# Performance work log

Hardware: AMD Instinct MI355X
Metric: run time of the kernel (lower is better)

Reference implementation:

```python
import jax, jax.numpy as jnp
import numpy as np

B = 16384       # batch
H = 512         # hidden_size
OUT = 4         # output_size (== GRU input_size)
FF = 2048       # MLP hidden width
HORIZON = 5     # prediction_horizon


def setup_inputs() -> dict:
    key = jax.random.key(0)
    ks = jax.random.split(key, 12)
    s = 0.05
    f32 = jnp.float32
    return {
        "predicted_values": jax.random.normal(ks[0], (B, HORIZON, OUT), f32),
        "past_time_features": jax.random.normal(ks[1], (B, H), f32),
        # nn.GRU (single layer) params, PyTorch layout: (3H, in) / (3H, H), gate order r,z,n
        "w_ih": jax.random.normal(ks[2], (3 * H, OUT), f32) * s,
        "w_hh": jax.random.normal(ks[3], (3 * H, H), f32) * s,
        "b_ih": jax.random.normal(ks[4], (3 * H,), f32) * s,
        "b_hh": jax.random.normal(ks[5], (3 * H,), f32) * s,
        # hx_fc: Linear(2H -> H)
        "w_fc": jax.random.normal(ks[6], (H, 2 * H), f32) * s,
        "b_fc": jax.random.normal(ks[7], (H,), f32) * s,
        # mlp: Linear(H -> 2048), Linear(2048 -> OUT); Dropout is identity at eval
        "w1": jax.random.normal(ks[8], (FF, H), f32) * s,
        "b1": jax.random.normal(ks[9], (FF,), f32) * s,
        "w2": jax.random.normal(ks[10], (OUT, FF), f32) * s,
        "b2": jax.random.normal(ks[11], (OUT,), f32) * s,
    }


def _gru_cell(x, h, w_ih, w_hh, b_ih, b_hh):
    # PyTorch GRU cell: gates ordered (r, z, n)
    gi = x @ w_ih.T + b_ih          # [B, 3H]
    gh = h @ w_hh.T + b_hh          # [B, 3H]
    i_r, i_z, i_n = jnp.split(gi, 3, axis=-1)
    h_r, h_z, h_n = jnp.split(gh, 3, axis=-1)
    r = jax.nn.sigmoid(i_r + h_r)
    z = jax.nn.sigmoid(i_z + h_z)
    n = jnp.tanh(i_n + r * h_n)
    return (1.0 - z) * n + z * h


def reference(predicted_values, past_time_features, w_ih, w_hh, b_ih, b_hh,
              w_fc, b_fc, w1, b1, w2, b2):
    b = predicted_values.shape[0]
    xy = jnp.zeros((b, OUT), predicted_values.dtype)
    hx = past_time_features.reshape(b, H)
    outs = []
    for i in range(HORIZON):
        # length-2 sequence through the GRU: [xy, predicted_values[:, i]]
        h1 = _gru_cell(xy, hx, w_ih, w_hh, b_ih, b_hh)
        h2 = _gru_cell(predicted_values[:, i, :], h1, w_ih, w_hh, b_ih, b_hh)
        hcat = jnp.concatenate([h1, h2], axis=-1)        # [B, 2H]
        hx = hcat @ w_fc.T + b_fc                        # [B, H]
        # MLP: ReLU -> Linear -> (Dropout=identity) -> ReLU -> Linear
        d_xy = jax.nn.relu(jax.nn.relu(hx) @ w1.T + b1) @ w2.T + b2
        xy = xy + d_xy
        outs.append(xy)
    return jnp.stack(outs, axis=1)                       # [B, HORIZON, OUT]
```

## Files before the change

### kernel.cpp

```cpp
#include <hip/hip_runtime.h>
#include <hip/hip_bf16.h>
#include <cstdint>
#include <cstddef>

#define Bsz 16384
#define HORsz 5

using bf16_t = __hip_bfloat16;
typedef __bf16 bf16x8 __attribute__((ext_vector_type(8)));
typedef float f32x4 __attribute__((ext_vector_type(4)));

__device__ __forceinline__ void gld_lds16(const void* g, void* l) {
  __builtin_amdgcn_global_load_lds((__attribute__((address_space(1))) void*)g,
                                   (__attribute__((address_space(3))) void*)l,
                                   16, 0, 0);
}

template <int N>
__device__ __forceinline__ void wait_vmcnt() {
  if constexpr (N == 0)      asm volatile("s_waitcnt vmcnt(0)" ::: "memory");
  else if constexpr (N == 3) asm volatile("s_waitcnt vmcnt(3)" ::: "memory");
  else if constexpr (N == 4) asm volatile("s_waitcnt vmcnt(4)" ::: "memory");
  else static_assert(N == 0 || N == 3 || N == 4, "unsupported vmcnt");
}

__device__ __forceinline__ float sigm(float x) { return 1.f / (1.f + __expf(-x)); }
__device__ __forceinline__ float tanh_fast(float x) {
  x = fminf(fmaxf(x, -20.f), 20.f);
  float e = __expf(2.f * x);
  return (e - 1.f) / (e + 1.f);
}

template <int CTRL>
__device__ __forceinline__ float dpp_add(float v) {
  int x = __builtin_amdgcn_update_dpp(0, __float_as_int(v), CTRL, 0xF, 0xF, true);
  return v + __int_as_float(x);
}
__device__ __forceinline__ float red16(float v) {
  v = dpp_add<0xB1>(v);
  v = dpp_add<0x4E>(v);
  v = dpp_add<0x124>(v);
  v = dpp_add<0x128>(v);
  return v;
}

__device__ __forceinline__ void swz(int b, int nbn, int& n, int& m) {
  const int x = b & 7;
  const int k = b >> 3;
  n = k % nbn;
  m = x + 8 * (k / nbn);
}

__device__ __forceinline__ size_t fl_off(int row, int col, int ca, int cofs) {
  return (size_t)((row >> 4) * ca + cofs + (col >> 5)) * 1024
       + (size_t)((((col >> 3) & 3) * 16 + (row & 15)) * 16 + (col & 7) * 2);
}

__global__ void __launch_bounds__(256) pack_fl(const float* __restrict__ src,
                                               char* __restrict__ dst,
                                               int C, int cs, int npieces) {
  const int p = blockIdx.x * 256 + threadIdx.x;
  if (p >= npieces) return;
  const int chunk = p >> 6, wi = p & 63;
  const int colgrp = wi >> 4, r15 = wi & 15;
  const int rowgrp = chunk >> cs, kg = chunk & ((1 << cs) - 1);
  const int row = rowgrp * 16 + r15;
  const int col = kg * 32 + colgrp * 8;
  const float* s = src + (size_t)row * C + col;
  bf16x8 v;
  #pragma unroll
  for (int j = 0; j < 8; ++j) v[j] = (__bf16)s[j];
  *(bf16x8*)(dst + (size_t)p * 16) = v;
}

__global__ void __launch_bounds__(256) pack_x(const float* __restrict__ src, int ld,
                                              char* __restrict__ dst, int ntot) {
  const int p = blockIdx.x * 256 + threadIdx.x;
  if (p >= ntot) return;
  const int slice = p >> 14, row = p & 16383;
  const float* s = src + (size_t)row * ld + slice * 4;
  bf16x8 v;
  v[0] = (__bf16)s[0]; v[1] = (__bf16)s[1]; v[2] = (__bf16)s[2]; v[3] = (__bf16)s[3];
  v[4] = (__bf16)1.0f; v[5] = (__bf16)0.f; v[6] = (__bf16)0.f; v[7] = (__bf16)0.f;
  char* base = dst + (size_t)slice * 1048576 + (size_t)(row >> 4) * 1024 + (row & 15) * 16;
  const bf16x8 z = {};
  *(bf16x8*)(base) = v;
  *(bf16x8*)(base + 256) = z;
  *(bf16x8*)(base + 512) = z;
  *(bf16x8*)(base + 768) = z;
}

__global__ void __launch_bounds__(256) pack_wih(const float* __restrict__ w_ih,
                                                const float* __restrict__ b_ih,
                                                const float* __restrict__ b_hh,
                                                char* __restrict__ dst) {
  const int row = blockIdx.x * 256 + threadIdx.x;
  if (row >= 1536) return;
  const float* s = w_ih + (size_t)row * 4;
  const float c4 = b_ih[row] + (row < 1024 ? b_hh[row] : 0.f);
  bf16x8 v;
  v[0] = (__bf16)s[0]; v[1] = (__bf16)s[1]; v[2] = (__bf16)s[2]; v[3] = (__bf16)s[3];
  v[4] = (__bf16)c4;   v[5] = (__bf16)0.f; v[6] = (__bf16)0.f; v[7] = (__bf16)0.f;
  char* base = dst + (size_t)(row >> 4) * 1024 + (row & 15) * 16;
  const bf16x8 z = {};
  *(bf16x8*)(base) = v;
  *(bf16x8*)(base + 256) = z;
  *(bf16x8*)(base + 512) = z;
  *(bf16x8*)(base + 768) = z;
}

__global__ void __launch_bounds__(256, 3) gru_fused7(
    const char* __restrict__ Afl, int ca,
    const char* __restrict__ Wfl,
    const char* __restrict__ xF,
    const char* __restrict__ wihF,
    const float* __restrict__ b_hh,
    char* __restrict__ Ofl, int co, int kofs)
{
  __shared__ char smem[36864];
  const int t = threadIdx.x, w = t >> 6, lane = t & 63;
  int bn, bm;
  swz(blockIdx.x, 8, bn, bm);
  const int m0 = bm * 64;
  const int n0 = bn * 64;

  const char* wsrc[3];
  const char* wsrc16[3];
  int loff[3];
  #pragma unroll
  for (int s = 0; s < 3; ++s) {
    const int c = w * 3 + s, g = c >> 2, cr = c & 3;
    wsrc[s]   = Wfl  + (size_t)(g * 32 + (n0 >> 4) + cr) * 16 * 1024 + lane * 16;
    wsrc16[s] = wihF + (size_t)(g * 32 + (n0 >> 4) + cr) * 1024 + lane * 16;
    loff[s] = c * 1024;
  }
  const char* asrc[4];
  const char* asrc16[4];
  #pragma unroll
  for (int i = 0; i < 4; ++i) {
    asrc[i]   = Afl + (size_t)((m0 >> 4) + i) * ca * 1024 + lane * 16;
    asrc16[i] = xF  + (size_t)((m0 >> 4) + i) * 1024 + lane * 16;
  }

  f32x4 acc[3][4], acc_ni[4];
  const f32x4 zero = {0.f, 0.f, 0.f, 0.f};
  #pragma unroll
  for (int g = 0; g < 3; ++g)
    #pragma unroll
    for (int i = 0; i < 4; ++i) acc[g][i] = zero;
  #pragma unroll
  for (int i = 0; i < 4; ++i) acc_ni[i] = zero;

  #pragma unroll
  for (int s = 0; s < 3; ++s)
    gld_lds16(wsrc[s], smem + loff[s]);
  #pragma unroll
  for (int s = 0; s < 3; ++s)
    gld_lds16(wsrc[s] + 1024, smem + 12288 + loff[s]);
  bf16x8 afC[4], afN[4];
  #pragma unroll
  for (int i = 0; i < 4; ++i)
    afC[i] = *(const bf16x8*)(asrc[i]);

  #pragma unroll
  for (int kg = 0; kg < 16; ++kg) {
    wait_vmcnt<3>();
    __builtin_amdgcn_s_barrier();
    __builtin_amdgcn_sched_barrier(0);
    const char* cur = smem + (kg % 3) * 12288;
    #pragma unroll
    for (int i = 0; i < 4; ++i)
      afN[i] = (kg + 1 < 16) ? *(const bf16x8*)(asrc[i] + (size_t)(kg + 1) * 1024)
                             : *(const bf16x8*)(asrc16[i]);
    if (kg + 2 <= 16) {
      char* nxt = smem + ((kg + 2) % 3) * 12288;
      #pragma unroll
      for (int s = 0; s < 3; ++s) {
        const char* src = (kg + 2 < 16) ? wsrc[s] + (size_t)(kg + 2) * 1024
                                        : wsrc16[s];
        gld_lds16(src, nxt + loff[s]);
      }
    }
    #pragma unroll
    for (int g = 0; g < 3; ++g) {
      const bf16x8 bv = *(const bf16x8*)(cur + (g * 4 + w) * 1024 + lane * 16);
      #pragma unroll
      for (int i = 0; i < 4; ++i)
        acc[g][i] = __builtin_amdgcn_mfma_f32_16x16x32_bf16(afC[i], bv, acc[g][i], 0, 0, 0);
    }
    #pragma unroll
    for (int i = 0; i < 4; ++i) afC[i] = afN[i];
  }

  wait_vmcnt<0>();
  __builtin_amdgcn_s_barrier();
  __builtin_amdgcn_sched_barrier(0);
  {
    const char* cur = smem + 12288;
    #pragma unroll
    for (int g = 0; g < 2; ++g) {
      const bf16x8 bv = *(const bf16x8*)(cur + (g * 4 + w) * 1024 + lane * 16);
      #pragma unroll
      for (int i = 0; i < 4; ++i)
        acc[g][i] = __builtin_amdgcn_mfma_f32_16x16x32_bf16(afC[i], bv, acc[g][i], 0, 0, 0);
    }
    const bf16x8 bv2 = *(const bf16x8*)(cur + (8 + w) * 1024 + lane * 16);
    #pragma unroll
    for (int i = 0; i < 4; ++i)
      acc_ni[i] = __builtin_amdgcn_mfma_f32_16x16x32_bf16(afC[i], bv2, acc_ni[i], 0, 0, 0);
  }

  const int lr = lane & 15, q4 = (lane >> 4) * 4;
  char* rep = smem + w * 2048;
  const int c = n0 + w * 16 + lr;
  const float bhn = b_hh[c + 1024];
  const int wbase = ((lr >> 3) * 16 + q4) * 16 + (lr & 7) * 2;
  #pragma unroll
  for (int i = 0; i < 4; ++i) {
    #pragma unroll
    for (int r4 = 0; r4 < 4; ++r4) {
      const int row = m0 + i * 16 + q4 + r4;
      const float rr = sigm(acc[0][i][r4]);
      const float zz = sigm(acc[1][i][r4]);
      const float nn = tanh_fast(acc_ni[i][r4] + rr * (acc[2][i][r4] + bhn));
      const float hp = (float)*(const __bf16*)(Afl + fl_off(row, c, ca, 0));
      *(__bf16*)(rep + i * 512 + wbase + r4 * 16) = (__bf16)((1.f - zz) * nn + zz * hp);
    }
  }
  const int rg0 = m0 >> 4;
  const int cg = kofs + (n0 >> 5) + (w >> 1);
  const int half = (w & 1) * 512;
  #pragma unroll
  for (int i = 0; i < 4; ++i) {
    const uint2 v = *(const uint2*)(rep + i * 512 + lane * 8);
    *(uint2*)(Ofl + ((size_t)(rg0 + i) * co + cg) * 1024 + half + lane * 8) = v;
  }
}

template <int NKG, int NJ, int MODE>
__global__ void __launch_bounds__(256, 4) gemm_fl5(
    const char* __restrict__ Afl,
    const char* __restrict__ Bfl, int nbn,
    const float* __restrict__ bias,
    char* __restrict__ O1, char* __restrict__ O2, int co,
    const float* __restrict__ w2, float* __restrict__ dxy)
{
  constexpr int NCH = 8 + 2 * NJ;
  constexpr int NS = NCH / 4;
  constexpr int BUFB = NCH * 1024;
  __shared__ char smem[2 * BUFB];
  const int t = threadIdx.x, w = t >> 6, lane = t & 63;
  int bn, bm;
  swz(blockIdx.x, nbn, bn, bm);
  const int m0 = bm * 128, n0 = bn * (NJ * 32);
  const int wm = (w >> 1) * 64, wn = (w & 1) * (NJ * 16);

  const char* gsrc[NS];
  int loff[NS];
  #pragma unroll
  for (int s = 0; s < NS; ++s) {
    const int idx = w * NS + s;
    if (idx < 8) gsrc[s] = Afl + (size_t)((m0 >> 4) + idx) * NKG * 1024 + lane * 16;
    else         gsrc[s] = Bfl + (size_t)((n0 >> 4) + idx - 8) * NKG * 1024 + lane * 16;
    loff[s] = idx * 1024;
  }

  f32x4 acc[4][NJ];
  const f32x4 zero = {0.f, 0.f, 0.f, 0.f};
  #pragma unroll
  for (int i = 0; i < 4; ++i)
    #pragma unroll
    for (int j = 0; j < NJ; ++j) acc[i][j] = zero;

  #pragma unroll
  for (int s = 0; s < NS; ++s)
    gld_lds16(gsrc[s], smem + loff[s]);

  #pragma unroll
  for (int kg = 0; kg < NKG; ++kg) {
    __syncthreads();
    const char* cur = smem + (kg & 1) * BUFB;
    if (kg + 1 < NKG) {
      char* nxt = smem + ((kg + 1) & 1) * BUFB;
      #pragma unroll
      for (int s = 0; s < NS; ++s)
        gld_lds16(gsrc[s] + (size_t)(kg + 1) * 1024, nxt + loff[s]);
    }
    bf16x8 af[4], bv[NJ];
    #pragma unroll
    for (int i = 0; i < 4; ++i)
      af[i] = *(const bf16x8*)(cur + ((wm >> 4) + i) * 1024 + lane * 16);
    #pragma unroll
    for (int j = 0; j < NJ; ++j)
      bv[j] = *(const bf16x8*)(cur + (8 + (wn >> 4) + j) * 1024 + lane * 16);
    #pragma unroll
    for (int i = 0; i < 4; ++i)
      #pragma unroll
      for (int j = 0; j < NJ; ++j)
        acc[i][j] = __builtin_amdgcn_mfma_f32_16x16x32_bf16(af[i], bv[j], acc[i][j], 0, 0, 0);
  }

  const int lr = lane & 15, q4 = (lane >> 4) * 4;
  if (MODE == 2) {
    char* rep = smem + w * (NJ / 2) * 1024;
    const int rgb = (m0 >> 4) + (wm >> 4);
    const int cgb = (n0 >> 5) + (wn >> 5);
    for (int i = 0; i < 4; ++i) {
      #pragma unroll
      for (int j = 0; j < NJ; ++j) {
        const int col = n0 + wn + j * 16 + lr;
        const float bvv = bias[col];
        const int wbase = (((j & 1) * 2 + (lr >> 3)) * 16 + q4) * 16 + (lr & 7) * 2;
        #pragma unroll
        for (int r = 0; r < 4; ++r) {
          const float v = acc[i][j][r] + bvv;
          *(__bf16*)(rep + (j >> 1) * 1024 + wbase + r * 16) = (__bf16)v;
        }
      }
      #pragma unroll
      for (int jc = 0; jc < NJ / 2; ++jc) {
        const bf16x8 v = *(const bf16x8*)(rep + jc * 1024 + lane * 16);
        const size_t cb = ((size_t)(rgb + i) * co + cgb + jc) * 1024 + lane * 16;
        *(bf16x8*)(O1 + cb) = v;
        bf16x8 vr;
        #pragma unroll
        for (int e = 0; e < 8; ++e) vr[e] = (__bf16)fmaxf((float)v[e], 0.f);
        *(bf16x8*)(O2 + cb) = vr;
      }
    }
  }
}

__global__ void __launch_bounds__(512, 2) mlp2b(
    const char* __restrict__ Afl,
    const char* __restrict__ Bfl,
    const float* __restrict__ bias,
    const float* __restrict__ w2,
    float* __restrict__ dxy)
{
  __shared__ char smem[2 * 32768];
  const int t = threadIdx.x, w = t >> 6, lane = t & 63;
  const int wr = w >> 2, wc = w & 3;
  int bn, bm;
  swz(blockIdx.x, 8, bn, bm);
  const int m0 = bm * 256, n0 = bn * 256;

  const char* gsrc[4];
  int loff[4];
  #pragma unroll
  for (int s = 0; s < 4; ++s) {
    const int idx = w * 4 + s;
    if (idx < 16) {
      gsrc[s] = Afl + (size_t)((m0 >> 4) + idx) * 16 * 1024 + lane * 16;
      loff[s] = idx * 1024;
    } else {
      gsrc[s] = Bfl + (size_t)((n0 >> 4) + idx - 16) * 16 * 1024 + lane * 16;
      loff[s] = 16384 + (idx - 16) * 1024;
    }
  }

  f32x4 acc[8][4];
  const f32x4 zero = {0.f, 0.f, 0.f, 0.f};
  #pragma unroll
  for (int i = 0; i < 8; ++i)
    #pragma unroll
    for (int j = 0; j < 4; ++j) acc[i][j] = zero;

  #pragma unroll
  for (int s = 0; s < 4; ++s)
    gld_lds16(gsrc[s], smem + loff[s]);

  #pragma unroll
  for (int kg = 0; kg < 16; ++kg) {
    __syncthreads();
    const char* cur = smem + (kg & 1) * 32768;
    if (kg + 1 < 16) {
      char* nxt = smem + ((kg + 1) & 1) * 32768;
      #pragma unroll
      for (int s = 0; s < 4; ++s)
        gld_lds16(gsrc[s] + (size_t)(kg + 1) * 1024, nxt + loff[s]);
    }
    bf16x8 af[8], bv[4];
    #pragma unroll
    for (int j = 0; j < 4; ++j)
      bv[j] = *(const bf16x8*)(cur + 16384 + (wc * 4 + j) * 1024 + lane * 16);
    #pragma unroll
    for (int i = 0; i < 8; ++i)
      af[i] = *(const bf16x8*)(cur + (wr * 8 + i) * 1024 + lane * 16);
    __builtin_amdgcn_s_setprio(1);
    #pragma unroll
    for (int i = 0; i < 8; ++i)
      #pragma unroll
      for (int j = 0; j < 4; ++j)
        acc[i][j] = __builtin_amdgcn_mfma_f32_16x16x32_bf16(af[i], bv[j], acc[i][j], 0, 0, 0);
    __builtin_amdgcn_s_setprio(0);
  }

  const int lr = lane & 15, q4 = (lane >> 4) * 4;
  const int slice = bn * 4 + wc;
  float bvv[4], w2c[4][4];
  #pragma unroll
  for (int j = 0; j < 4; ++j) {
    const int col = n0 + wc * 64 + j * 16 + lr;
    bvv[j] = bias[col];
    w2c[j][0] = w2[col];        w2c[j][1] = w2[2048 + col];
    w2c[j][2] = w2[4096 + col]; w2c[j][3] = w2[6144 + col];
  }
  #pragma unroll
  for (int i = 0; i < 8; ++i) {
    float v[4][4];
    #pragma unroll
    for (int r = 0; r < 4; ++r)
      #pragma unroll
      for (int o = 0; o < 4; ++o) v[r][o] = 0.f;
    #pragma unroll
    for (int j = 0; j < 4; ++j) {
      #pragma unroll
      for (int r = 0; r < 4; ++r) {
        const float pv = fmaxf(acc[i][j][r] + bvv[j], 0.f);
        v[r][0] += pv * w2c[j][0]; v[r][1] += pv * w2c[j][1];
        v[r][2] += pv * w2c[j][2]; v[r][3] += pv * w2c[j][3];
      }
    }
    #pragma unroll
    for (int r = 0; r < 4; ++r)
      #pragma unroll
      for (int o = 0; o < 4; ++o) v[r][o] = red16(v[r][o]);
    if (lr == 0) {
      #pragma unroll
      for (int r = 0; r < 4; ++r) {
        const int row = m0 + wr * 128 + i * 16 + q4 + r;
        float4 vv = make_float4(v[r][0], v[r][1], v[r][2], v[r][3]);
        *(float4*)(dxy + ((size_t)slice * Bsz + row) * 4) = vv;
      }
    }
  }
}

__global__ void __launch_bounds__(256) finalize(
    const float* __restrict__ dxy, const float* __restrict__ b2,
    float* __restrict__ xy, float* __restrict__ out, int istep,
    char* __restrict__ xyF)
{
  const int b = blockIdx.x * 256 + threadIdx.x;
  float4 s = *(const float4*)b2;
  #pragma unroll 8
  for (int sl = 0; sl < 32; ++sl) {
    const float4 d = *(const float4*)(dxy + ((size_t)sl * Bsz + b) * 4);
    s.x += d.x; s.y += d.y; s.z += d.z; s.w += d.w;
  }
  float4 xv = *(const float4*)(xy + (size_t)b * 4);
  xv.x += s.x; xv.y += s.y; xv.z += s.z; xv.w += s.w;
  *(float4*)(xy + (size_t)b * 4) = xv;
  *(float4*)(out + (size_t)b * 20 + istep * 4) = xv;
  bf16x8 v;
  v[0] = (__bf16)xv.x; v[1] = (__bf16)xv.y; v[2] = (__bf16)xv.z; v[3] = (__bf16)xv.w;
  v[4] = (__bf16)1.0f; v[5] = (__bf16)0.f; v[6] = (__bf16)0.f; v[7] = (__bf16)0.f;
  *(bf16x8*)(xyF + (size_t)(b >> 4) * 1024 + (b & 15) * 16) = v;
}

extern "C" void kernel_launch(void* const* d_in, const int* in_sizes, int n_in,
                              void* d_out, int out_size, void* d_ws, size_t ws_size,
                              hipStream_t stream)
{
  const float* pv   = (const float*)d_in[0];
  const float* ptf  = (const float*)d_in[1];
  const float* w_ih = (const float*)d_in[2];
  const float* w_hh = (const float*)d_in[3];
  const float* b_ih = (const float*)d_in[4];
  const float* b_hh = (const float*)d_in[5];
  const float* w_fc = (const float*)d_in[6];
  const float* b_fc = (const float*)d_in[7];
  const float* w1   = (const float*)d_in[8];
  const float* b1   = (const float*)d_in[9];
  const float* w2   = (const float*)d_in[10];
  const float* b2   = (const float*)d_in[11];
  float* out = (float*)d_out;

  char* p = (char*)d_ws;
  auto carve = [&](size_t bytes) {
    char* r = p;
    p += (bytes + 255) & ~(size_t)255;
    return r;
  };
  char*  hxF   = carve((size_t)Bsz * 512 * 2);
  char*  hxrF  = carve((size_t)Bsz * 512 * 2);
  char*  hcatF = carve((size_t)Bsz * 1024 * 2);
  float* dxy   = (float*)carve((size_t)32 * Bsz * 4 * 4);
  float* xy    = (float*)carve((size_t)Bsz * 4 * 4);
  char*  whhF  = carve((size_t)1536 * 512 * 2);
  char*  wfcF  = carve((size_t)512 * 1024 * 2);
  char*  w1F   = carve((size_t)2048 * 512 * 2);
  char*  xyF   = carve((size_t)1024 * 1024);
  char*  pvF   = carve((size_t)5 * 1024 * 1024);
  char*  wihF  = carve((size_t)96 * 1024);

  pack_fl<<<(1536 * 512 / 8 + 255) / 256, 256, 0, stream>>>(w_hh, whhF, 512, 4, 1536 * 512 / 8);
  pack_fl<<<(512 * 1024 / 8 + 255) / 256, 256, 0, stream>>>(w_fc, wfcF, 1024, 5, 512 * 1024 / 8);
  pack_fl<<<(2048 * 512 / 8 + 255) / 256, 256, 0, stream>>>(w1, w1F, 512, 4, 2048 * 512 / 8);
  pack_fl<<<(Bsz * 512 / 8 + 255) / 256, 256, 0, stream>>>(ptf, hxF, 512, 4, Bsz * 512 / 8);
  pack_wih<<<6, 256, 0, stream>>>(w_ih, b_ih, b_hh, wihF);
  pack_x<<<(Bsz * HORsz + 255) / 256, 256, 0, stream>>>(pv, HORsz * 4, pvF, Bsz * HORsz);
  hipMemsetAsync(xy, 0, (size_t)Bsz * 4 * 4, stream);
  pack_x<<<Bsz / 256, 256, 0, stream>>>(xy, 4, xyF, Bsz);

  for (int i = 0; i < HORsz; ++i) {
    gru_fused7<<<2048, 256, 0, stream>>>(
        hxF, 16, whhF, xyF, wihF, b_hh, hcatF, 32, 0);
    gru_fused7<<<2048, 256, 0, stream>>>(
        hcatF, 32, whhF, pvF + (size_t)i * 1048576, wihF, b_hh, hcatF, 32, 16);
    gemm_fl5<32, 2, 2><<<1024, 256, 0, stream>>>(
        hcatF, wfcF, 8, b_fc, hxF, hxrF, 16, nullptr, nullptr);
    mlp2b<<<512, 512, 0, stream>>>(hxrF, w1F, b1, w2, dxy);
    finalize<<<Bsz / 256, 256, 0, stream>>>(dxy, b2, xy, out, i, xyF);
  }
}
```

Before: 865.5 us.

## Switch GRU kernel to double-buffered LDS to raise occupancy

The GRU GEMM kernel's weight staging drops from a three-stage LDS ring with fine-grained vmcnt waits to a two-buffer scheme using __syncthreads. Shared memory falls from 36 KB to 24 KB and the launch bound now asks for 4 blocks per CU instead of 3. The epilogue scratch area moves to the second buffer so it does not overlap the last tile being read. The aim is more resident waves to hide memory latency. In exchange, prefetch distance shrinks to one stage and the full barrier drains outstanding loads each iteration, which may expose load latency.

```diff
diff --git a/kernel.cpp b/kernel.cpp
--- a/kernel.cpp
+++ b/kernel.cpp
@@ -14,14 +14,6 @@
   __builtin_amdgcn_global_load_lds((__attribute__((address_space(1))) void*)g,
                                    (__attribute__((address_space(3))) void*)l,
                                    16, 0, 0);
-}
-
-template <int N>
-__device__ __forceinline__ void wait_vmcnt() {
-  if constexpr (N == 0)      asm volatile("s_waitcnt vmcnt(0)" ::: "memory");
-  else if constexpr (N == 3) asm volatile("s_waitcnt vmcnt(3)" ::: "memory");
-  else if constexpr (N == 4) asm volatile("s_waitcnt vmcnt(4)" ::: "memory");
-  else static_assert(N == 0 || N == 3 || N == 4, "unsupported vmcnt");
 }
 
 __device__ __forceinline__ float sigm(float x) { return 1.f / (1.f + __expf(-x)); }
@@ -109,7 +101,7 @@
   *(bf16x8*)(base + 768) = z;
 }
 
-__global__ void __launch_bounds__(256, 3) gru_fused7(
+__global__ void __launch_bounds__(256, 4) gru_fused9(
     const char* __restrict__ Afl, int ca,
     const char* __restrict__ Wfl,
     const char* __restrict__ xF,
@@ -117,7 +109,7 @@
     const float* __restrict__ b_hh,
     char* __restrict__ Ofl, int co, int kofs)
 {
-  __shared__ char smem[36864];
+  __shared__ char smem[24576];
   const int t = threadIdx.x, w = t >> 6, lane = t & 63;
   int bn, bm;
   swz(blockIdx.x, 8, bn, bm);
@@ -154,9 +146,6 @@
   #pragma unroll
   for (int s = 0; s < 3; ++s)
     gld_lds16(wsrc[s], smem + loff[s]);
-  #pragma unroll
-  for (int s = 0; s < 3; ++s)
-    gld_lds16(wsrc[s] + 1024, smem + 12288 + loff[s]);
   bf16x8 afC[4], afN[4];
   #pragma unroll
   for (int i = 0; i < 4; ++i)
@@ -164,23 +153,21 @@
 
   #pragma unroll
   for (int kg = 0; kg < 16; ++kg) {
-    wait_vmcnt<3>();
-    __builtin_amdgcn_s_barrier();
-    __builtin_amdgcn_sched_barrier(0);
-    const char* cur = smem + (kg % 3) * 12288;
+    __syncthreads();
+    const char* cur = smem + (kg & 1) * 12288;
+    {
+      char* nxt = smem + ((kg + 1) & 1) * 12288;
+      #pragma unroll
+      for (int s = 0; s < 3; ++s) {
+        const char* src = (kg + 1 < 16) ? wsrc[s] + (size_t)(kg + 1) * 1024
+                                        : wsrc16[s];
+        gld_lds16(src, nxt + loff[s]);
+      }
+    }
     #pragma unroll
     for (int i = 0; i < 4; ++i)
       afN[i] = (kg + 1 < 16) ? *(const bf16x8*)(asrc[i] + (size_t)(kg + 1) * 1024)
                              : *(const bf16x8*)(asrc16[i]);
-    if (kg + 2 <= 16) {
-      char* nxt = smem + ((kg + 2) % 3) * 12288;
-      #pragma unroll
-      for (int s = 0; s < 3; ++s) {
-        const char* src = (kg + 2 < 16) ? wsrc[s] + (size_t)(kg + 2) * 1024
-                                        : wsrc16[s];
-        gld_lds16(src, nxt + loff[s]);
-      }
-    }
     #pragma unroll
     for (int g = 0; g < 3; ++g) {
       const bf16x8 bv = *(const bf16x8*)(cur + (g * 4 + w) * 1024 + lane * 16);
@@ -192,11 +179,9 @@
     for (int i = 0; i < 4; ++i) afC[i] = afN[i];
   }
 
-  wait_vmcnt<0>();
-  __builtin_amdgcn_s_barrier();
-  __builtin_amdgcn_sched_barrier(0);
+  __syncthreads();
   {
-    const char* cur = smem + 12288;
+    const char* cur = smem;
     #pragma unroll
     for (int g = 0; g < 2; ++g) {
       const bf16x8 bv = *(const bf16x8*)(cur + (g * 4 + w) * 1024 + lane * 16);
@@ -211,7 +196,7 @@
   }
 
   const int lr = lane & 15, q4 = (lane >> 4) * 4;
-  char* rep = smem + w * 2048;
+  char* rep = smem + 12288 + w * 2048;
   const int c = n0 + w * 16 + lr;
   const float bhn = b_hh[c + 1024];
   const int wbase = ((lr >> 3) * 16 + q4) * 16 + (lr & 7) * 2;
@@ -505,9 +490,9 @@
   pack_x<<<Bsz / 256, 256, 0, stream>>>(xy, 4, xyF, Bsz);
 
   for (int i = 0; i < HORsz; ++i) {
-    gru_fused7<<<2048, 256, 0, stream>>>(
+    gru_fused9<<<2048, 256, 0, stream>>>(
         hxF, 16, whhF, xyF, wihF, b_hh, hcatF, 32, 0);
-    gru_fused7<<<2048, 256, 0, stream>>>(
+    gru_fused9<<<2048, 256, 0, stream>>>(
         hcatF, 32, whhF, pvF + (size_t)i * 1048576, wihF, b_hh, hcatF, 32, 16);
     gemm_fl5<32, 2, 2><<<1024, 256, 0, stream>>>(
         hcatF, wfcF, 8, b_fc, hxF, hxrF, 16, nullptr, nullptr);
```

Result: faster. 848.0 us (-2.0%).
